# Optimization experiments

Measured on AMD Instinct MI355X. Metric: run time of the kernel, lower is better.

Reference implementation:

```python
import jax, jax.numpy as jnp
import numpy as np

N_HOPS = 2
N_ENTITIES = 100000
EMB = 64
N_REL = 32
N_EDGES = 1000000


def _l2norm(x, eps=1e-12):
    # torch F.normalize: x / max(||x||_2, eps) per row
    n = jnp.sqrt(jnp.sum(x * x, axis=1, keepdims=True))
    return x / jnp.maximum(n, eps)


def setup_inputs() -> dict:
    key = jax.random.key(0)
    k1, k2, k3, k4, k5, k6 = jax.random.split(key, 6)
    return {
        "entity_emb": jax.random.normal(k1, (N_ENTITIES, EMB), dtype=jnp.float32),
        "edge_emb": jax.random.normal(k2, (N_REL, EMB), dtype=jnp.float32) * 0.1,
        "q_w": jax.random.normal(k3, (EMB, EMB), dtype=jnp.float32) * (1.0 / np.sqrt(EMB)),
        "k_w": jax.random.normal(k4, (EMB, EMB), dtype=jnp.float32) * (1.0 / np.sqrt(EMB)),
        "edge_index": jax.random.randint(k5, (2, N_EDGES), 0, N_ENTITIES, dtype=jnp.int32),
        "edge_type": jax.random.randint(k6, (N_EDGES,), 0, N_REL, dtype=jnp.int32),
        "mess_dropout": 0,
    }


def reference(entity_emb, edge_emb, q_w, k_w, edge_index, edge_type, mess_dropout):
    head = edge_index[0]
    tail = edge_index[1]
    rel = edge_emb[edge_type]                      # [E, D]
    kg = jnp.zeros_like(entity_emb)
    agg = entity_emb
    for _ in range(N_HOPS):
        # edge-wise tanh attention score
        left = (agg @ q_w)[head]                   # [E, D] (factor GEMM out of gather)
        right = jnp.tanh((rel * agg[tail]) @ k_w)  # [E, D]
        att = jnp.sum(left * right, axis=1)        # [E]
        # scatter_softmax over head segments
        m = jax.ops.segment_max(att, head, num_segments=N_ENTITIES)
        e = jnp.exp(att - jax.lax.stop_gradient(m)[head])
        denom = jax.ops.segment_sum(e, head, num_segments=N_ENTITIES)
        w = e / denom[head]                        # [E]
        # weighted messages + scatter_mean aggregation
        msg = w[:, None] * rel * agg[tail]         # [E, D]
        s = jax.ops.segment_sum(msg, head, num_segments=N_ENTITIES)
        cnt = jax.ops.segment_sum(jnp.ones_like(w), head, num_segments=N_ENTITIES)
        agg = s / jnp.maximum(cnt, 1.0)[:, None]
        # mess_dropout=False path; normalize + residual accumulation
        agg = _l2norm(agg)
        kg = kg + agg + entity_emb
    return kg
```

## Files before the change

kernel.cpp:

```cpp
#include <hip/hip_runtime.h>
#include <math.h>

#define EMB 64
#define MAXREL 32
#define BSHIFT 9
#define BCAP 6912
#define CH 2048

typedef short bf16x8 __attribute__((ext_vector_type(8)));
typedef float f32x4 __attribute__((ext_vector_type(4)));

__device__ __forceinline__ short f2bf(float f) {
    unsigned u = __float_as_uint(f);
    u += 0x7FFFu + ((u >> 16) & 1u);
    return (short)(u >> 16);
}

#if __has_builtin(__builtin_amdgcn_cvt_pk_bf16_f32)
__device__ __forceinline__ short2 cvt2(float a, float b) {
    return __builtin_bit_cast(short2, __builtin_amdgcn_cvt_pk_bf16_f32(a, b));
}
#else
__device__ __forceinline__ short2 cvt2(float a, float b) {
    return make_short2(f2bf(a), f2bf(b));
}
#endif

__device__ __forceinline__ float lo_bf(unsigned d) { return __uint_as_float(d << 16); }
__device__ __forceinline__ float hi_bf(unsigned d) { return __uint_as_float(d & 0xffff0000u); }
__device__ __forceinline__ float bfs(short s) {
    return __uint_as_float(((unsigned)(unsigned short)s) << 16);
}

__device__ __forceinline__ bf16x8 pack8bf(uint4 U, float4 r0, float4 r1) {
    short2 c0 = cvt2(lo_bf(U.x) * r0.x, hi_bf(U.x) * r0.y);
    short2 c1 = cvt2(lo_bf(U.y) * r0.z, hi_bf(U.y) * r0.w);
    short2 c2 = cvt2(lo_bf(U.z) * r1.x, hi_bf(U.z) * r1.y);
    short2 c3 = cvt2(lo_bf(U.w) * r1.z, hi_bf(U.w) * r1.w);
    bf16x8 a;
    a[0] = c0.x; a[1] = c0.y; a[2] = c1.x; a[3] = c1.y;
    a[4] = c2.x; a[5] = c2.y; a[6] = c3.x; a[7] = c3.y;
    return a;
}

__device__ __forceinline__ float fast_rcp(float x) {
#if __has_builtin(__builtin_amdgcn_rcpf)
    return __builtin_amdgcn_rcpf(x);
#else
    return 1.0f / x;
#endif
}

__device__ __forceinline__ float fast_tanh(float x) {
    float ax = fabsf(x);
    float z = __expf(2.0f * ax);
    float r = 1.0f - 2.0f * fast_rcp(z + 1.0f);
    return copysignf(r, x);
}

__global__ void init_kernel(short4* __restrict__ aggbf, float4* __restrict__ kg,
                            const float4* __restrict__ ent, int n4) {
    int i = blockIdx.x * blockDim.x + threadIdx.x;
    if (i < n4) {
        float4 v = ent[i];
        short2 c0 = cvt2(v.x, v.y), c1 = cvt2(v.z, v.w);
        aggbf[i] = make_short4(c0.x, c0.y, c1.x, c1.y);
        kg[i] = make_float4(0.f, 0.f, 0.f, 0.f);
    }
}


__global__ void hist_kernel(int* __restrict__ deg, const int* __restrict__ head, int E) {
    int e = blockIdx.x * blockDim.x + threadIdx.x;
    if (e < E) atomicAdd(&deg[head[e]], 1);
}

__global__ void scan_blocks(const int* __restrict__ deg, int* __restrict__ excl,
                            int* __restrict__ bsum, int n) {
    __shared__ int wsum[4];
    int base = blockIdx.x * 1024;
    int t = threadIdx.x;
    int lane = t & 63, wid = t >> 6;
    int idx = base + t * 4;
    int v0 = (idx + 0 < n) ? deg[idx + 0] : 0;
    int v1 = (idx + 1 < n) ? deg[idx + 1] : 0;
    int v2 = (idx + 2 < n) ? deg[idx + 2] : 0;
    int v3 = (idx + 3 < n) ? deg[idx + 3] : 0;
    int s0 = v0, s1 = s0 + v1, s2 = s1 + v2, s3 = s2 + v3;
    int tsum = s3;
    int inc = tsum;
#pragma unroll
    for (int o = 1; o < 64; o <<= 1) { int u = __shfl_up(inc, o, 64); if (lane >= o) inc += u; }
    if (lane == 63) wsum[wid] = inc;
    __syncthreads();
    int woff = 0;
#pragma unroll
    for (int w = 0; w < 4; ++w) if (w < wid) woff += wsum[w];
    int texcl = woff + inc - tsum;
    if (idx + 0 < n) excl[idx + 0] = texcl;
    if (idx + 1 < n) excl[idx + 1] = texcl + s0;
    if (idx + 2 < n) excl[idx + 2] = texcl + s1;
    if (idx + 3 < n) excl[idx + 3] = texcl + s2;
    if (t == 255) bsum[blockIdx.x] = woff + inc;
}

__global__ void scan_sums(int* __restrict__ bsum, int* __restrict__ excl, int nb, int n, int E) {
    __shared__ int ws[4];
    int t = threadIdx.x;
    if (nb > 256) {
        if (t == 0) {
            int acc = 0;
            for (int b = 0; b < nb; ++b) { int v = bsum[b]; bsum[b] = acc; acc += v; }
            excl[n] = E;
        }
        return;
    }
    int lane = t & 63, wid = t >> 6;
    int v = (t < nb) ? bsum[t] : 0;
    int inc = v;
#pragma unroll
    for (int o = 1; o < 64; o <<= 1) { int u = __shfl_up(inc, o, 64); if (lane >= o) inc += u; }
    if (lane == 63) ws[wid] = inc;
    __syncthreads();
    int woff = 0;
#pragma unroll
    for (int w = 0; w < 4; ++w) if (w < wid) woff += ws[w];
    if (t < nb) bsum[t] = woff + inc - v;
    if (t == 0) excl[n] = E;
}

__global__ void scan_add(int* __restrict__ excl, const int* __restrict__ bsum,
                         int* __restrict__ bcursor, int n) {
    int i = blockIdx.x * blockDim.x + threadIdx.x;
    if (i < n) {
        int v = excl[i] + bsum[i >> 10];
        excl[i] = v;
        if ((i & ((1 << BSHIFT) - 1)) == 0) bcursor[i >> BSHIFT] = v;
    }
}

__global__ void bucket_scatter(const int* __restrict__ head, const int* __restrict__ tail,
                               const int* __restrict__ etype, int* __restrict__ bcursor,
                               int2* __restrict__ tmp, int E, int nb) {
    __shared__ int lcnt[512];
    __shared__ int lbase[512];
    int t = threadIdx.x;
    int base = blockIdx.x * CH;
    for (int i = t; i < 512; i += 256) lcnt[i] = 0;
    __syncthreads();
    int myh[8];
#pragma unroll
    for (int i = 0; i < 8; ++i) {
        int e = base + i * 256 + t;
        if (e < E) {
            int h = head[e];
            myh[i] = h;
            atomicAdd(&lcnt[h >> BSHIFT], 1);
        } else myh[i] = -1;
    }
    __syncthreads();
    for (int b = t; b < nb; b += 256) {
        int c = lcnt[b];
        lbase[b] = (c > 0) ? atomicAdd(&bcursor[b], c) : 0;
        lcnt[b] = 0;
    }
    __syncthreads();
#pragma unroll
    for (int i = 0; i < 8; ++i) {
        int e = base + i * 256 + t;
        if (e < E) {
            int h = myh[i];
            int b = h >> BSHIFT;
            int pos = lbase[b] + atomicAdd(&lcnt[b], 1);
            tmp[pos] = make_int2(h, tail[e] | (etype[e] << 20));
        }
    }
}

__global__ void bucket_sort(const int* __restrict__ offsets, const int2* __restrict__ tmp,
                            int2* __restrict__ spair, int N) {
    __shared__ int2 staged[BCAP];
    __shared__ int lcur[1 << BSHIFT];
    int b = blockIdx.x;
    int h0 = b << BSHIFT;
    int h1 = min(h0 + (1 << BSHIFT), N);
    int r0 = offsets[h0], r1 = offsets[h1];
    int cnt = r1 - r0;
    int t = threadIdx.x;
    for (int h = h0 + t; h < h1; h += blockDim.x) lcur[h - h0] = offsets[h] - r0;
    __syncthreads();
    if (cnt <= BCAP) {
        for (int i = t; i < cnt; i += blockDim.x) {
            int2 rec = tmp[r0 + i];
            int lp = atomicAdd(&lcur[rec.x - h0], 1);
            staged[lp] = rec;
        }
        __syncthreads();
        for (int i = t; i < cnt; i += blockDim.x) spair[r0 + i] = staged[i];
    } else {
        for (int i = t; i < cnt; i += blockDim.x) {
            int2 rec = tmp[r0 + i];
            int lp = atomicAdd(&lcur[rec.x - h0], 1);
            spair[r0 + lp] = rec;
        }
    }
}


__device__ __forceinline__ void build_bfrags(bf16x8 bfrag[2][4], const float* __restrict__ W,
                                             int lane) {
    int koff = (lane >> 4) * 8;
    int n = lane & 15;
#pragma unroll
    for (int kh = 0; kh < 2; ++kh)
#pragma unroll
        for (int nt = 0; nt < 4; ++nt) {
            bf16x8 b;
#pragma unroll
            for (int j = 0; j < 8; ++j)
                b[j] = f2bf(W[(kh * 32 + koff + j) * EMB + nt * 16 + n]);
            bfrag[kh][nt] = b;
        }
}

__global__ void qproj_mfma_kernel(short* __restrict__ Qbf, const short* __restrict__ aggbf,
                                  const float* __restrict__ qw, int N) {
    int lane = threadIdx.x & 63;
    int gwave = blockIdx.x * (blockDim.x >> 6) + (threadIdx.x >> 6);
    int nwaves = gridDim.x * (blockDim.x >> 6);
    int row = lane & 15;
    int g = lane >> 4;
    int koff = g * 8;

    bf16x8 bfrag[2][4];
    build_bfrags(bfrag, qw, lane);

    int ntiles = (N + 15) >> 4;
    for (int tile = gwave; tile < ntiles; tile += nwaves) {
        int rIdx = min(tile * 16 + row, N - 1);
        const short* rowp = aggbf + (size_t)rIdx * EMB;
        bf16x8 a0 = *(const bf16x8*)(rowp + koff);
        bf16x8 a1 = *(const bf16x8*)(rowp + 32 + koff);
#pragma unroll
        for (int nt = 0; nt < 4; ++nt) {
            f32x4 acc = {0.f, 0.f, 0.f, 0.f};
            acc = __builtin_amdgcn_mfma_f32_16x16x32_bf16(a0, bfrag[0][nt], acc, 0, 0, 0);
            acc = __builtin_amdgcn_mfma_f32_16x16x32_bf16(a1, bfrag[1][nt], acc, 0, 0, 0);
#pragma unroll
            for (int reg = 0; reg < 4; ++reg) {
                int n2 = tile * 16 + g * 4 + reg;
                if (n2 < N) Qbf[(size_t)n2 * EMB + nt * 16 + (lane & 15)] = f2bf(acc[reg]);
            }
        }
    }
}

__global__ void att_mfma_kernel(float* __restrict__ att,
                                const short* __restrict__ aggbf, const short* __restrict__ Qbf,
                                const float* __restrict__ eemb, const float* __restrict__ kw,
                                const int2* __restrict__ spair, int E) {
    int lane = threadIdx.x & 63;
    int gwave = blockIdx.x * (blockDim.x >> 6) + (threadIdx.x >> 6);
    int nwaves = gridDim.x * (blockDim.x >> 6);
    int row = lane & 15;
    int g = lane >> 4;

    bf16x8 bfrag[2][4];
    build_bfrags(bfrag, kw, lane);

    int ntiles = (E + 15) >> 4;
    int tile = gwave;
    int2 pr = make_int2(0, 0);
    uint4 U0 = make_uint4(0, 0, 0, 0), U1 = make_uint4(0, 0, 0, 0);
    if (tile < ntiles) {
        pr = spair[min(tile * 16 + row, E - 1)];
        const uint4* rowa = (const uint4*)(aggbf + (size_t)(pr.y & 0xFFFFF) * EMB);
        U0 = rowa[g];
        U1 = rowa[4 + g];
    }
    for (; tile < ntiles; tile += nwaves) {
        int tnext = tile + nwaves;
        int2 prn = pr;
        if (tnext < ntiles) prn = spair[min(tnext * 16 + row, E - 1)];

        int h = pr.x;
        unsigned r = ((unsigned)pr.y) >> 20;
        const float4* rl4 = (const float4*)(eemb + (size_t)r * EMB);
        float4 y0 = rl4[g * 2], y1 = rl4[g * 2 + 1];
        float4 y2 = rl4[8 + g * 2], y3 = rl4[8 + g * 2 + 1];
        bf16x8 a0 = pack8bf(U0, y0, y1);
        bf16x8 a1 = pack8bf(U1, y2, y3);

        uint4 U0n = U0, U1n = U1;
        if (tnext < ntiles) {
            const uint4* rowan = (const uint4*)(aggbf + (size_t)(prn.y & 0xFFFFF) * EMB);
            U0n = rowan[g];
            U1n = rowan[4 + g];
        }

        int h2r0 = __shfl(h, g * 4 + 0, 64);
        int h2r1 = __shfl(h, g * 4 + 1, 64);
        int h2r2 = __shfl(h, g * 4 + 2, 64);
        int h2r3 = __shfl(h, g * 4 + 3, 64);
        const short* q0 = Qbf + (size_t)h2r0 * EMB + (lane & 15);
        const short* q1 = Qbf + (size_t)h2r1 * EMB + (lane & 15);
        const short* q2 = Qbf + (size_t)h2r2 * EMB + (lane & 15);
        const short* q3 = Qbf + (size_t)h2r3 * EMB + (lane & 15);

        float sums0 = 0.f, sums1 = 0.f, sums2 = 0.f, sums3 = 0.f;
#pragma unroll
        for (int nt = 0; nt < 4; ++nt) {
            f32x4 acc = {0.f, 0.f, 0.f, 0.f};
            acc = __builtin_amdgcn_mfma_f32_16x16x32_bf16(a0, bfrag[0][nt], acc, 0, 0, 0);
            acc = __builtin_amdgcn_mfma_f32_16x16x32_bf16(a1, bfrag[1][nt], acc, 0, 0, 0);
            sums0 += bfs(q0[nt * 16]) * fast_tanh(acc[0]);
            sums1 += bfs(q1[nt * 16]) * fast_tanh(acc[1]);
            sums2 += bfs(q2[nt * 16]) * fast_tanh(acc[2]);
            sums3 += bfs(q3[nt * 16]) * fast_tanh(acc[3]);
        }
#pragma unroll
        for (int m = 1; m <= 8; m <<= 1) {
            sums0 += __shfl_xor(sums0, m, 64);
            sums1 += __shfl_xor(sums1, m, 64);
            sums2 += __shfl_xor(sums2, m, 64);
            sums3 += __shfl_xor(sums3, m, 64);
        }
#pragma unroll
        for (int reg = 0; reg < 4; ++reg) {
            int row2 = g * 4 + reg;
            int e2 = tile * 16 + row2;
            float v = (reg == 0) ? sums0 : (reg == 1) ? sums1 : (reg == 2) ? sums2 : sums3;
            if ((lane & 15) == reg && e2 < E) att[e2] = v;
        }
        pr = prn; U0 = U0n; U1 = U1n;
    }
}

__global__ void head_agg_kernel(short* __restrict__ aggNewBf, float* __restrict__ kg,
                                const float* __restrict__ att, const short* __restrict__ aggOldBf,
                                const float* __restrict__ eemb, const float* __restrict__ ent,
                                const int* __restrict__ offsets, const int2* __restrict__ spair,
                                int N, int R) {
    __shared__ float4 elds4[MAXREL * 16];

    int tid = threadIdx.x;
    int lane = tid & 63;
    int wid = tid >> 6;
    int RS = (R < MAXREL) ? R : MAXREL;
    for (int i = tid; i < RS * 16; i += blockDim.x) elds4[i] = ((const float4*)eemb)[i];
    __syncthreads();

    int sub = lane >> 4;
    int q = lane & 15;
    int h = (blockIdx.x * (blockDim.x >> 6) + wid) * 4 + sub;
    if (h >= N) return;
    int beg = offsets[h], end = offsets[h + 1];
    int deg = end - beg;

    float m = -3.4e38f;
    for (int e = beg + q; e < end; e += 16) m = fmaxf(m, att[e]);
#pragma unroll
    for (int o = 1; o <= 8; o <<= 1) m = fmaxf(m, __shfl_xor(m, o, 64));

    float4 acc4 = make_float4(0.f, 0.f, 0.f, 0.f);
    float ssum = 0.f;
    int qbase = lane & 48;
    for (int c = beg; c < end; c += 16) {
        int e = c + q;
        float ev = 0.f; int tr = 0;
        if (e < end) {
            ev = __expf(att[e] - m);
            tr = spair[e].y;
        }
        ssum += ev;
        int nc = min(16, end - c);
        auto body = [&](int j) {
            int src = qbase | j;
            float ej = __shfl(ev, src, 64);
            int trj = __shfl(tr, src, 64);
            int tj = trj & 0xFFFFF;
            unsigned rj = ((unsigned)trj) >> 20;
            float4 ew = (rj < (unsigned)RS) ? elds4[rj * 16 + q]
                                            : ((const float4*)eemb)[(size_t)rj * 16 + q];
            uint2 X = ((const uint2*)(aggOldBf + (size_t)tj * EMB))[q];
            acc4.x += ej * ew.x * lo_bf(X.x);
            acc4.y += ej * ew.y * hi_bf(X.x);
            acc4.z += ej * ew.z * lo_bf(X.y);
            acc4.w += ej * ew.w * hi_bf(X.y);
        };
        if (nc == 16) {
#pragma unroll 4
            for (int j = 0; j < 16; ++j) body(j);
        } else {
            int j = 0;
            for (; j + 4 <= nc; j += 4) {
                body(j); body(j + 1); body(j + 2); body(j + 3);
            }
            for (; j < nc; ++j) body(j);
        }
    }
#pragma unroll
    for (int o = 1; o <= 8; o <<= 1) ssum += __shfl_xor(ssum, o, 64);

    float scale = (deg > 0) ? 1.0f / (ssum * (float)deg) : 0.f;
    float4 v = make_float4(acc4.x * scale, acc4.y * scale, acc4.z * scale, acc4.w * scale);
    float ss = v.x * v.x + v.y * v.y + v.z * v.z + v.w * v.w;
#pragma unroll
    for (int o = 1; o <= 8; o <<= 1) ss += __shfl_xor(ss, o, 64);
    float rinv = 1.0f / fmaxf(sqrtf(ss), 1e-12f);
    v.x *= rinv; v.y *= rinv; v.z *= rinv; v.w *= rinv;

    short2 c0 = cvt2(v.x, v.y), c1 = cvt2(v.z, v.w);
    ((short4*)aggNewBf)[(size_t)h * 16 + q] = make_short4(c0.x, c0.y, c1.x, c1.y);
    float4 kgv = ((float4*)kg)[(size_t)h * 16 + q];
    float4 ev2 = ((const float4*)ent)[(size_t)h * 16 + q];
    kgv.x += v.x + ev2.x; kgv.y += v.y + ev2.y;
    kgv.z += v.z + ev2.z; kgv.w += v.w + ev2.w;
    ((float4*)kg)[(size_t)h * 16 + q] = kgv;
}

extern "C" void kernel_launch(void* const* d_in, const int* in_sizes, int n_in,
                              void* d_out, int out_size, void* d_ws, size_t ws_size,
                              hipStream_t stream) {
    const float* ent  = (const float*)d_in[0];
    const float* eemb = (const float*)d_in[1];
    const float* qw   = (const float*)d_in[2];
    const float* kw   = (const float*)d_in[3];
    const int* eidx  = (const int*)d_in[4];
    const int* etype = (const int*)d_in[5];

    const int N = in_sizes[0] / EMB;
    const int R = in_sizes[1] / EMB;
    const int E = in_sizes[5];
    const int* head = eidx;
    const int* tail = eidx + E;

    float* kg = (float*)d_out;

    float* att   = (float*)d_ws;
    int2* spair  = (int2*)(att + E);
    int* offsets = (int*)(spair + E);
    int* deg     = offsets + (N + 1);
    int* bcursor = deg + N;
    int* bsum    = bcursor + N;
    uintptr_t pa = ((uintptr_t)(bsum + 1024) + 15) & ~(uintptr_t)15;
    short* aggbf_a = (short*)pa;
    short* aggbf_b = aggbf_a + (size_t)N * EMB;
    short* Qbf     = aggbf_b + (size_t)N * EMB;
    int2* tmp      = (int2*)Qbf;

    const int NT = 256;
    const int nb = (N + 1023) / 1024;
    const int nbk = (N + (1 << BSHIFT) - 1) >> BSHIFT;

    init_kernel<<<(N * EMB / 4 + NT - 1) / NT, NT, 0, stream>>>(
        (short4*)aggbf_a, (float4*)kg, (const float4*)ent, N * EMB / 4);
    hipMemsetAsync(deg, 0, (size_t)N * 4, stream);
    hist_kernel<<<(E + NT - 1) / NT, NT, 0, stream>>>(deg, head, E);
    scan_blocks<<<nb, NT, 0, stream>>>(deg, offsets, bsum, N);
    scan_sums<<<1, NT, 0, stream>>>(bsum, offsets, nb, N, E);
    scan_add<<<(N + NT - 1) / NT, NT, 0, stream>>>(offsets, bsum, bcursor, N);
    bucket_scatter<<<(E + CH - 1) / CH, NT, 0, stream>>>(head, tail, etype, bcursor, tmp, E, nbk);
    bucket_sort<<<nbk, NT, 0, stream>>>(offsets, tmp, spair, N);

    short* curbf = aggbf_a;
    short* nxtbf = aggbf_b;
    for (int hop = 0; hop < 2; ++hop) {
        qproj_mfma_kernel<<<512, NT, 0, stream>>>(Qbf, curbf, qw, N);
        att_mfma_kernel<<<2048, NT, 0, stream>>>(att, curbf, Qbf, eemb, kw, spair, E);
        head_agg_kernel<<<(N + 15) / 16, NT, 0, stream>>>(nxtbf, kg, att, curbf,
                                                          eemb, ent, offsets, spair, N, R);
        short* ts = curbf; curbf = nxtbf; nxtbf = ts;
    }
}
```

Measured before the change: 417.5 us.

## Fuse attention scoring and head aggregation into one per-head-block kernel

Merges the edge attention MFMA kernel and the head softmax/aggregation kernel into one kernel. Each 512-thread block owns 32 consecutive heads, computes attention for their contiguous sorted edges, and keeps the scores in LDS unless they exceed 1024, in which case it falls back to global memory. This removes one launch and the global round trip of the attention array, and the tail rows are read twice close together, so cache reuse should improve. In exchange it drops the cross-tile prefetch of tail rows, adds a block barrier, and can leave waves unevenly loaded when degrees are skewed.

```diff
diff --git a/kernel.cpp b/kernel.cpp
--- a/kernel.cpp
+++ b/kernel.cpp
@@ -6,6 +6,8 @@
 #define BSHIFT 9
 #define BCAP 6912
 #define CH 2048
+#define HPB 32
+#define LCAP 1024
 
 typedef short bf16x8 __attribute__((ext_vector_type(8)));
 typedef float f32x4 __attribute__((ext_vector_type(4)));
@@ -255,57 +257,60 @@
     }
 }
 
-__global__ void att_mfma_kernel(float* __restrict__ att,
-                                const short* __restrict__ aggbf, const short* __restrict__ Qbf,
-                                const float* __restrict__ eemb, const float* __restrict__ kw,
-                                const int2* __restrict__ spair, int E) {
-    int lane = threadIdx.x & 63;
-    int gwave = blockIdx.x * (blockDim.x >> 6) + (threadIdx.x >> 6);
-    int nwaves = gridDim.x * (blockDim.x >> 6);
+__global__ __launch_bounds__(512) void fused_hop_kernel(
+        short* __restrict__ aggNewBf, float* __restrict__ kg,
+        float* __restrict__ attg,
+        const short* __restrict__ aggbf, const short* __restrict__ Qbf,
+        const float* __restrict__ eemb, const float* __restrict__ kw,
+        const float* __restrict__ ent,
+        const int* __restrict__ offsets, const int2* __restrict__ spair,
+        int N, int R) {
+    __shared__ float4 elds4[MAXREL * 16];
+    __shared__ float attl[LCAP];
+
+    int tid = threadIdx.x;
+    int lane = tid & 63;
+    int wid = tid >> 6;
+    int RS = (R < MAXREL) ? R : MAXREL;
+    for (int i = tid; i < RS * 16; i += blockDim.x) elds4[i] = ((const float4*)eemb)[i];
+
+    bf16x8 bfrag[2][4];
+    build_bfrags(bfrag, kw, lane);
+
+    int h0 = blockIdx.x * HPB;
+    int h1 = min(h0 + HPB, N);
+    int beg = offsets[h0], end = offsets[h1];
+    int cnt = end - beg;
+    bool inl = (cnt <= LCAP);
+    __syncthreads();
+
     int row = lane & 15;
     int g = lane >> 4;
-
-    bf16x8 bfrag[2][4];
-    build_bfrags(bfrag, kw, lane);
-
-    int ntiles = (E + 15) >> 4;
-    int tile = gwave;
-    int2 pr = make_int2(0, 0);
-    uint4 U0 = make_uint4(0, 0, 0, 0), U1 = make_uint4(0, 0, 0, 0);
-    if (tile < ntiles) {
-        pr = spair[min(tile * 16 + row, E - 1)];
-        const uint4* rowa = (const uint4*)(aggbf + (size_t)(pr.y & 0xFFFFF) * EMB);
-        U0 = rowa[g];
-        U1 = rowa[4 + g];
-    }
-    for (; tile < ntiles; tile += nwaves) {
-        int tnext = tile + nwaves;
-        int2 prn = pr;
-        if (tnext < ntiles) prn = spair[min(tnext * 16 + row, E - 1)];
-
+    int ntiles = (cnt + 15) >> 4;
+    for (int tile = wid; tile < ntiles; tile += 8) {
+        int e0 = beg + tile * 16;
+        int eld = min(e0 + row, end - 1);
+        int2 pr = spair[eld];
         int h = pr.x;
+        int t = pr.y & 0xFFFFF;
         unsigned r = ((unsigned)pr.y) >> 20;
+        const uint4* rowa = (const uint4*)(aggbf + (size_t)t * EMB);
         const float4* rl4 = (const float4*)(eemb + (size_t)r * EMB);
+        uint4 U0 = rowa[g];
+        uint4 U1 = rowa[4 + g];
         float4 y0 = rl4[g * 2], y1 = rl4[g * 2 + 1];
         float4 y2 = rl4[8 + g * 2], y3 = rl4[8 + g * 2 + 1];
         bf16x8 a0 = pack8bf(U0, y0, y1);
         bf16x8 a1 = pack8bf(U1, y2, y3);
 
-        uint4 U0n = U0, U1n = U1;
-        if (tnext < ntiles) {
-            const uint4* rowan = (const uint4*)(aggbf + (size_t)(prn.y & 0xFFFFF) * EMB);
-            U0n = rowan[g];
-            U1n = rowan[4 + g];
-        }
-
         int h2r0 = __shfl(h, g * 4 + 0, 64);
         int h2r1 = __shfl(h, g * 4 + 1, 64);
         int h2r2 = __shfl(h, g * 4 + 2, 64);
         int h2r3 = __shfl(h, g * 4 + 3, 64);
-        const short* q0 = Qbf + (size_t)h2r0 * EMB + (lane & 15);
-        const short* q1 = Qbf + (size_t)h2r1 * EMB + (lane & 15);
-        const short* q2 = Qbf + (size_t)h2r2 * EMB + (lane & 15);
-        const short* q3 = Qbf + (size_t)h2r3 * EMB + (lane & 15);
+        const short* q0 = Qbf + (size_t)h2r0 * EMB + row;
+        const short* q1 = Qbf + (size_t)h2r1 * EMB + row;
+        const short* q2 = Qbf + (size_t)h2r2 * EMB + row;
+        const short* q3 = Qbf + (size_t)h2r3 * EMB + row;
 
         float sums0 = 0.f, sums1 = 0.f, sums2 = 0.f, sums3 = 0.f;
 #pragma unroll
@@ -327,53 +332,42 @@
         }
 #pragma unroll
         for (int reg = 0; reg < 4; ++reg) {
-            int row2 = g * 4 + reg;
-            int e2 = tile * 16 + row2;
+            int e2 = e0 + g * 4 + reg;
             float v = (reg == 0) ? sums0 : (reg == 1) ? sums1 : (reg == 2) ? sums2 : sums3;
-            if ((lane & 15) == reg && e2 < E) att[e2] = v;
-        }
-        pr = prn; U0 = U0n; U1 = U1n;
-    }
-}
-
-__global__ void head_agg_kernel(short* __restrict__ aggNewBf, float* __restrict__ kg,
-                                const float* __restrict__ att, const short* __restrict__ aggOldBf,
-                                const float* __restrict__ eemb, const float* __restrict__ ent,
-                                const int* __restrict__ offsets, const int2* __restrict__ spair,
-                                int N, int R) {
-    __shared__ float4 elds4[MAXREL * 16];
-
-    int tid = threadIdx.x;
-    int lane = tid & 63;
-    int wid = tid >> 6;
-    int RS = (R < MAXREL) ? R : MAXREL;
-    for (int i = tid; i < RS * 16; i += blockDim.x) elds4[i] = ((const float4*)eemb)[i];
+            if (row == reg && e2 < end) {
+                if (inl) attl[e2 - beg] = v;
+                else attg[e2] = v;
+            }
+        }
+    }
     __syncthreads();
 
     int sub = lane >> 4;
     int q = lane & 15;
-    int h = (blockIdx.x * (blockDim.x >> 6) + wid) * 4 + sub;
+    int h = h0 + wid * 4 + sub;
     if (h >= N) return;
-    int beg = offsets[h], end = offsets[h + 1];
-    int deg = end - beg;
+    int hbeg = offsets[h], hend = offsets[h + 1];
+    int deg = hend - hbeg;
 
     float m = -3.4e38f;
-    for (int e = beg + q; e < end; e += 16) m = fmaxf(m, att[e]);
+    if (inl) { for (int e = hbeg + q; e < hend; e += 16) m = fmaxf(m, attl[e - beg]); }
+    else     { for (int e = hbeg + q; e < hend; e += 16) m = fmaxf(m, attg[e]); }
 #pragma unroll
     for (int o = 1; o <= 8; o <<= 1) m = fmaxf(m, __shfl_xor(m, o, 64));
 
     float4 acc4 = make_float4(0.f, 0.f, 0.f, 0.f);
     float ssum = 0.f;
     int qbase = lane & 48;
-    for (int c = beg; c < end; c += 16) {
+    for (int c = hbeg; c < hend; c += 16) {
         int e = c + q;
         float ev = 0.f; int tr = 0;
-        if (e < end) {
-            ev = __expf(att[e] - m);
+        if (e < hend) {
+            float av = inl ? attl[e - beg] : attg[e];
+            ev = __expf(av - m);
             tr = spair[e].y;
         }
         ssum += ev;
-        int nc = min(16, end - c);
+        int nc = min(16, hend - c);
         auto body = [&](int j) {
             int src = qbase | j;
             float ej = __shfl(ev, src, 64);
@@ -382,7 +376,7 @@
             unsigned rj = ((unsigned)trj) >> 20;
             float4 ew = (rj < (unsigned)RS) ? elds4[rj * 16 + q]
                                             : ((const float4*)eemb)[(size_t)rj * 16 + q];
-            uint2 X = ((const uint2*)(aggOldBf + (size_t)tj * EMB))[q];
+            uint2 X = ((const uint2*)(aggbf + (size_t)tj * EMB))[q];
             acc4.x += ej * ew.x * lo_bf(X.x);
             acc4.y += ej * ew.y * hi_bf(X.x);
             acc4.z += ej * ew.z * lo_bf(X.y);
@@ -465,11 +459,11 @@
 
     short* curbf = aggbf_a;
     short* nxtbf = aggbf_b;
+    const int nfb = (N + HPB - 1) / HPB;
     for (int hop = 0; hop < 2; ++hop) {
         qproj_mfma_kernel<<<512, NT, 0, stream>>>(Qbf, curbf, qw, N);
-        att_mfma_kernel<<<2048, NT, 0, stream>>>(att, curbf, Qbf, eemb, kw, spair, E);
-        head_agg_kernel<<<(N + 15) / 16, NT, 0, stream>>>(nxtbf, kg, att, curbf,
-                                                          eemb, ent, offsets, spair, N, R);
+        fused_hop_kernel<<<nfb, 512, 0, stream>>>(nxtbf, kg, att, curbf, Qbf, eemb, kw,
+                                                  ent, offsets, spair, N, R);
         short* ts = curbf; curbf = nxtbf; nxtbf = ts;
     }
 }
```

Measured after the change: 463.3 us. 1.11x slower.
